# Performance work log

Hardware: AMD Instinct MI355X
Metric: run time of the kernel (lower is better)

The kernel has to match this reference:

```python
import jax, jax.numpy as jnp
import numpy as np

N_GROUPS = 32
N_HEADS = 16
EPS = 1e-5


def group_norm(x, w, b):
    # x: [B, C, T]
    B, C, T = x.shape
    xg = x.reshape(B, N_GROUPS, C // N_GROUPS, T)
    mu = xg.mean(axis=(2, 3), keepdims=True)
    var = xg.var(axis=(2, 3), keepdims=True)
    xn = ((xg - mu) * jax.lax.rsqrt(var + EPS)).reshape(B, C, T)
    return xn * w[None, :, None] + b[None, :, None]


def setup_inputs() -> dict:
    key = jax.random.key(0)
    ks = jax.random.split(key, 5)
    B, C, T = 4, 1024, 1024
    return {
        "x": jax.random.normal(ks[0], (B, C, T), jnp.float32),
        "norm_weight": jnp.ones((C,), jnp.float32),
        "norm_bias": jnp.zeros((C,), jnp.float32),
        "qkv_w": jax.random.normal(ks[1], (3 * C, C), jnp.float32) * 0.02,
        "qkv_b": jax.random.normal(ks[2], (3 * C,), jnp.float32) * 0.02,
        "proj_w": jax.random.normal(ks[3], (C, C), jnp.float32) * 0.02,
        "proj_b": jax.random.normal(ks[4], (C,), jnp.float32) * 0.02,
    }


def reference(x, norm_weight, norm_bias, qkv_w, qkv_b, proj_w, proj_b):
    B, C, T = x.shape
    H = N_HEADS
    ch = C // H
    # GroupNorm + 1x1 conv to QKV: [B, 3C, T]
    xn = group_norm(x, norm_weight, norm_bias)
    qkv = jnp.einsum('oc,bct->bot', qkv_w, xn) + qkv_b[None, :, None]
    # Legacy layout: [B, H*3*ch, T] -> [B, H, 3, ch, T]
    qkv = qkv.reshape(B, H, 3, ch, T)
    q, k, v = qkv[:, :, 0], qkv[:, :, 1], qkv[:, :, 2]
    scale = 1.0 / jnp.sqrt(jnp.sqrt(jnp.asarray(ch, x.dtype)))
    w = jnp.einsum('bhct,bhcs->bhts', q * scale, k * scale)
    w = jax.nn.softmax(w.astype(jnp.float32), axis=-1).astype(w.dtype)
    a = jnp.einsum('bhts,bhcs->bhct', w, v).reshape(B, C, T)
    h = jnp.einsum('oc,bct->bot', proj_w, a) + proj_b[None, :, None]
    return x + h
```

## Files before the change

### kernel.cpp

```cpp
#include <hip/hip_runtime.h>
#include <hip/hip_bf16.h>

typedef __bf16 bf16;
typedef bf16  bf16x4 __attribute__((ext_vector_type(4)));
typedef bf16  bf16x8 __attribute__((ext_vector_type(8)));
typedef float f32x4  __attribute__((ext_vector_type(4)));

union B8 { bf16x8 v; bf16 e[8]; };
union B4 { bf16x4 v; bf16 e[4]; };
union F4 { f32x4 v; float e[4]; };

#define GLOAD_LDS16(g, l)                                            \
  __builtin_amdgcn_global_load_lds(                                  \
      (const __attribute__((address_space(1))) void*)(g),            \
      (__attribute__((address_space(3))) void*)(l), 16, 0, 0)

#define SWZ(arr, R, c8) (*(const bf16x8*)&(arr)[(size_t)(R) * 64 + (((c8) ^ ((R) & 7)) << 3)])

__global__ __launch_bounds__(256) void conv_w_kernel(
    const float* __restrict__ qkvw, const float* __restrict__ qkvb,
    const float* __restrict__ pw,
    bf16* __restrict__ Wb, bf16* __restrict__ Pb, float* __restrict__ bs)
{
  const int row = blockIdx.x;
  const int tid = threadIdx.x;
  if (row < 3072) {
    const float s = ((row % 192) < 128) ? 0.42468158f : 1.0f;
    const float4 a = ((const float4*)(qkvw + (size_t)row * 1024))[tid];
    B4 o;
    o.e[0] = (bf16)(a.x * s); o.e[1] = (bf16)(a.y * s);
    o.e[2] = (bf16)(a.z * s); o.e[3] = (bf16)(a.w * s);
    ((bf16x4*)(Wb + (size_t)row * 1024))[tid] = o.v;
    if (tid == 0) bs[row] = qkvb[row] * s;
  } else {
    const int r = row - 3072;
    const float4 a = ((const float4*)(pw + (size_t)r * 1024))[tid];
    B4 o;
    o.e[0] = (bf16)a.x; o.e[1] = (bf16)a.y;
    o.e[2] = (bf16)a.z; o.e[3] = (bf16)a.w;
    ((bf16x4*)(Pb + (size_t)r * 1024))[tid] = o.v;
  }
}

__global__ __launch_bounds__(256) void gn_t_kernel(
    const float* __restrict__ x, const float* __restrict__ w,
    const float* __restrict__ bias, bf16* __restrict__ xnt)
{
  const int blk = blockIdx.x;
  const int b = blk >> 5, g = blk & 31;
  const float* xp = x + (size_t)(b * 1024 + g * 32) * 1024;
  const int tid = threadIdx.x;

  float s = 0.f, ss = 0.f;
  for (int ch = tid; ch < 4096; ch += 256) {
    const float4* p = (const float4*)(xp + (size_t)ch * 8);
    float4 u0 = p[0], u1 = p[1];
    s  += u0.x + u0.y + u0.z + u0.w + u1.x + u1.y + u1.z + u1.w;
    ss += u0.x*u0.x + u0.y*u0.y + u0.z*u0.z + u0.w*u0.w
        + u1.x*u1.x + u1.y*u1.y + u1.z*u1.z + u1.w*u1.w;
  }
  #pragma unroll
  for (int m = 1; m < 64; m <<= 1) { s += __shfl_xor(s, m); ss += __shfl_xor(ss, m); }

  __shared__ float red[8];
  __shared__ float stats[2];
  const int wave = tid >> 6, lane = tid & 63;
  if (lane == 0) { red[wave] = s; red[4 + wave] = ss; }
  __syncthreads();
  if (tid == 0) {
    float ts  = red[0] + red[1] + red[2] + red[3];
    float tss = red[4] + red[5] + red[6] + red[7];
    float mu  = ts * (1.f / 32768.f);
    float var = tss * (1.f / 32768.f) - mu * mu;
    stats[0] = mu;
    stats[1] = rsqrtf(var + 1e-5f);
  }
  __syncthreads();
  const float mu = stats[0], rs = stats[1];

  for (int ti = 0; ti < 4; ++ti) {
    const int t = ti * 256 + tid;
    B8 o[4];
    #pragma unroll
    for (int cc = 0; cc < 32; ++cc) {
      const float wt = w[g * 32 + cc] * rs;
      const float bsv = bias[g * 32 + cc];
      const float v = xp[(size_t)cc * 1024 + t];
      o[cc >> 3].e[cc & 7] = (bf16)((v - mu) * wt + bsv);
    }
    bf16* dst = xnt + (size_t)(b * 1024 + t) * 1024 + g * 32;
    #pragma unroll
    for (int j = 0; j < 4; ++j) *(bf16x8*)(dst + j * 8) = o[j].v;
  }
}

__global__ __launch_bounds__(256) void gemm_qkv_kernel(
    const bf16* __restrict__ xnt, const bf16* __restrict__ Wb,
    const float* __restrict__ bs, bf16* __restrict__ qkT, bf16* __restrict__ vv)
{
  const int bx = blockIdx.x;
  const int t0 = blockIdx.y * 128, z = blockIdx.z;
  const bf16* Ab = xnt + (size_t)z * 1024 * 1024;
  const bf16* Bb = Wb + (size_t)bx * 128 * 1024;

  __shared__ __align__(16) bf16 Al[128 * 64];
  __shared__ __align__(16) bf16 Bl[128 * 64];

  const int tid  = threadIdx.x;
  const int wave = tid >> 6, lane = tid & 63;
  const int quad = lane >> 4, l15 = lane & 15;
  const int wr = wave >> 1, wc = wave & 1;
  const int lrow = lane >> 3, lp = lane & 7;

  F4 acc[4][4];
  #pragma unroll
  for (int i = 0; i < 4; ++i)
    #pragma unroll
    for (int j = 0; j < 4; ++j) acc[i][j].v = (f32x4){0.f, 0.f, 0.f, 0.f};

  for (int k0 = 0; k0 < 1024; k0 += 64) {
    #pragma unroll
    for (int call = 0; call < 4; ++call) {
      const int row = wave * 32 + call * 8 + lrow;
      const int c8  = lp ^ (row & 7);
      GLOAD_LDS16(Ab + (size_t)(t0 + row) * 1024 + k0 + c8 * 8,
                  &Al[(wave * 32 + call * 8) * 64]);
      GLOAD_LDS16(Bb + (size_t)row * 1024 + k0 + c8 * 8,
                  &Bl[(wave * 32 + call * 8) * 64]);
    }
    __syncthreads();

    #pragma unroll
    for (int ks = 0; ks < 2; ++ks) {
      bf16x8 af[4], bfr[4];
      #pragma unroll
      for (int mt = 0; mt < 4; ++mt)
        af[mt] = SWZ(Al, wr * 64 + mt * 16 + l15, ks * 4 + quad);
      #pragma unroll
      for (int nt = 0; nt < 4; ++nt)
        bfr[nt] = SWZ(Bl, wc * 64 + nt * 16 + l15, ks * 4 + quad);
      #pragma unroll
      for (int mt = 0; mt < 4; ++mt)
        #pragma unroll
        for (int nt = 0; nt < 4; ++nt)
          acc[mt][nt].v = __builtin_amdgcn_mfma_f32_16x16x32_bf16(
              af[mt], bfr[nt], acc[mt][nt].v, 0, 0, 0);
    }
    __syncthreads();
  }

  #pragma unroll
  for (int nt = 0; nt < 4; ++nt) {
    const int base = bx * 128 + wc * 64 + nt * 16;
    const int r192 = base % 192, head = base / 192;
    const float bb = bs[base + l15];
    if (r192 < 128) {
      const size_t col = head * 128 + r192 + l15;
      #pragma unroll
      for (int mt = 0; mt < 4; ++mt)
        #pragma unroll
        for (int r = 0; r < 4; ++r) {
          const int t = t0 + wr * 64 + mt * 16 + quad * 4 + r;
          qkT[(size_t)(z * 1024 + t) * 2048 + col] = (bf16)(acc[mt][nt].e[r] + bb);
        }
    } else {
      bf16* vrow = vv + ((size_t)z * 1024 + head * 64 + (r192 - 128) + l15) * 1024;
      #pragma unroll
      for (int mt = 0; mt < 4; ++mt) {
        const int t = t0 + wr * 64 + mt * 16 + quad * 4;
        B4 pk;
        #pragma unroll
        for (int r = 0; r < 4; ++r) pk.e[r] = (bf16)(acc[mt][nt].e[r] + bb);
        *(bf16x4*)&vrow[t] = pk.v;
      }
    }
  }
}

__global__ __launch_bounds__(256) void gemm_proj_kernel(
    const bf16* __restrict__ Pb, const bf16* __restrict__ Bt,
    float* __restrict__ Cf, const float* __restrict__ bias,
    const float* __restrict__ resf)
{
  const int z = blockIdx.z;
  Bt   += (size_t)z * 1024 * 1024;
  Cf   += (size_t)z * 1024 * 1024;
  resf += (size_t)z * 1024 * 1024;
  const int n0 = blockIdx.x * 64, m0 = blockIdx.y * 64;

  __shared__ __align__(16) bf16 Al[64 * 64];
  __shared__ __align__(16) bf16 Bl[64 * 64];

  const int tid  = threadIdx.x;
  const int wave = tid >> 6, lane = tid & 63;
  const int quad = lane >> 4, l15 = lane & 15;
  const int wr = wave >> 1, wc = wave & 1;
  const int lrow = lane >> 3, lp = lane & 7;

  F4 acc[2][2];
  #pragma unroll
  for (int i = 0; i < 2; ++i)
    #pragma unroll
    for (int j = 0; j < 2; ++j) acc[i][j].v = (f32x4){0.f, 0.f, 0.f, 0.f};

  for (int k0 = 0; k0 < 1024; k0 += 64) {
    #pragma unroll
    for (int call = 0; call < 2; ++call) {
      const int row = wave * 16 + call * 8 + lrow;
      const int c8  = lp ^ (row & 7);
      GLOAD_LDS16(Pb + (size_t)(m0 + row) * 1024 + k0 + c8 * 8,
                  &Al[(wave * 16 + call * 8) * 64]);
      GLOAD_LDS16(Bt + (size_t)(n0 + row) * 1024 + k0 + c8 * 8,
                  &Bl[(wave * 16 + call * 8) * 64]);
    }
    __syncthreads();

    #pragma unroll
    for (int ks = 0; ks < 2; ++ks) {
      bf16x8 af[2], bfr[2];
      #pragma unroll
      for (int mt = 0; mt < 2; ++mt)
        af[mt] = SWZ(Al, wr * 32 + mt * 16 + l15, ks * 4 + quad);
      #pragma unroll
      for (int nt = 0; nt < 2; ++nt)
        bfr[nt] = SWZ(Bl, wc * 32 + nt * 16 + l15, ks * 4 + quad);
      #pragma unroll
      for (int mt = 0; mt < 2; ++mt)
        #pragma unroll
        for (int nt = 0; nt < 2; ++nt)
          acc[mt][nt].v = __builtin_amdgcn_mfma_f32_16x16x32_bf16(
              af[mt], bfr[nt], acc[mt][nt].v, 0, 0, 0);
    }
    __syncthreads();
  }

  #pragma unroll
  for (int mt = 0; mt < 2; ++mt) {
    #pragma unroll
    for (int r = 0; r < 4; ++r) {
      const int m = m0 + wr * 32 + mt * 16 + quad * 4 + r;
      const float bb = bias[m];
      #pragma unroll
      for (int nt = 0; nt < 2; ++nt) {
        const int n = n0 + wc * 32 + nt * 16 + l15;
        Cf[(size_t)m * 1024 + n] = acc[mt][nt].e[r] + bb + resf[(size_t)m * 1024 + n];
      }
    }
  }
}

__global__ __launch_bounds__(256) void attn_kernel(
    const bf16* __restrict__ qkTin, const bf16* __restrict__ vmat,
    bf16* __restrict__ aout)
{
  const int h = blockIdx.x, tt = blockIdx.y, z = blockIdx.z;
  const bf16* qk = qkTin + (size_t)z * 1024 * 2048;
  const bf16* vp = vmat + (size_t)z * 1024 * 1024 + (size_t)(h * 64) * 1024;
  aout += (size_t)z * 1024 * 1024;
  const int t0 = tt * 128;

  __shared__ __align__(16) bf16 qP[128 * 64];
  __shared__ __align__(16) bf16 kl[2][64 * 64];
  __shared__ __align__(16) bf16 vl[2][64 * 64];

  const int tid  = threadIdx.x;
  const int wave = tid >> 6, lane = tid & 63;
  const int quad = lane >> 4, l15 = lane & 15;
  const int lrow = lane >> 3, lp = lane & 7;

  #pragma unroll
  for (int c = 0; c < 4; ++c) {
    const int row = wave * 32 + c * 8 + lrow;
    const int c8  = lp ^ (row & 7);
    GLOAD_LDS16(qk + (size_t)(t0 + row) * 2048 + h * 128 + c8 * 8,
                &qP[(wave * 32 + c * 8) * 64]);
  }
  const int r0 = wave * 16 + lrow, r1 = wave * 16 + 8 + lrow;
  const int c80 = lp ^ (r0 & 7), c81 = lp ^ (r1 & 7);
  GLOAD_LDS16(qk + (size_t)r0 * 2048 + h * 128 + 64 + c80 * 8, &kl[0][(wave * 16) * 64]);
  GLOAD_LDS16(qk + (size_t)r1 * 2048 + h * 128 + 64 + c81 * 8, &kl[0][(wave * 16 + 8) * 64]);
  GLOAD_LDS16(vp + (size_t)r0 * 1024 + c80 * 8, &vl[0][(wave * 16) * 64]);
  GLOAD_LDS16(vp + (size_t)r1 * 1024 + c81 * 8, &vl[0][(wave * 16 + 8) * 64]);
  __syncthreads();

  bf16x8 bq0[2], bq1[2];
  int prow[2];
  #pragma unroll
  for (int b = 0; b < 2; ++b) {
    const int Rq = wave * 32 + b * 16 + l15;
    bq0[b] = SWZ(qP, Rq, quad);
    bq1[b] = SWZ(qP, Rq, quad + 4);
    prow[b] = Rq;
  }

  float l_i[2] = {0.f, 0.f};
  F4 oacc[2][4];
  #pragma unroll
  for (int b = 0; b < 2; ++b)
    #pragma unroll
    for (int ct = 0; ct < 4; ++ct) oacc[b][ct].v = (f32x4){0.f, 0.f, 0.f, 0.f};

  const int pq8 = (quad & 1) * 4;

  int buf = 0;
  for (int s0 = 0; s0 < 1024; s0 += 64) {
    if (s0 + 64 < 1024) {
      const int nb = buf ^ 1, sn = s0 + 64;
      GLOAD_LDS16(qk + (size_t)(sn + r0) * 2048 + h * 128 + 64 + c80 * 8,
                  &kl[nb][(wave * 16) * 64]);
      GLOAD_LDS16(qk + (size_t)(sn + r1) * 2048 + h * 128 + 64 + c81 * 8,
                  &kl[nb][(wave * 16 + 8) * 64]);
      GLOAD_LDS16(vp + (size_t)r0 * 1024 + sn + c80 * 8, &vl[nb][(wave * 16) * 64]);
      GLOAD_LDS16(vp + (size_t)r1 * 1024 + sn + c81 * 8, &vl[nb][(wave * 16 + 8) * 64]);
    }

    bf16x8 ak0[4], ak1[4], bv[2][4];
    #pragma unroll
    for (int st = 0; st < 4; ++st) {
      const int Rk = st * 16 + l15;
      ak0[st] = SWZ(kl[buf], Rk, quad);
      ak1[st] = SWZ(kl[buf], Rk, quad + 4);
    }
    #pragma unroll
    for (int ks = 0; ks < 2; ++ks)
      #pragma unroll
      for (int ct = 0; ct < 4; ++ct)
        bv[ks][ct] = SWZ(vl[buf], ct * 16 + l15, ks * 4 + quad);

    #pragma unroll
    for (int b = 0; b < 2; ++b) {
      F4 sacc[4];
      #pragma unroll
      for (int st = 0; st < 4; ++st) sacc[st].v = (f32x4){0.f, 0.f, 0.f, 0.f};
      #pragma unroll
      for (int st = 0; st < 4; ++st) {
        sacc[st].v = __builtin_amdgcn_mfma_f32_16x16x32_bf16(ak0[st], bq0[b], sacc[st].v, 0, 0, 0);
        sacc[st].v = __builtin_amdgcn_mfma_f32_16x16x32_bf16(ak1[st], bq1[b], sacc[st].v, 0, 0, 0);
      }

      bf16* const pbase = &qP[(size_t)prow[b] * 64];
      #pragma unroll
      for (int st = 0; st < 4; ++st) {
        B4 pk;
        #pragma unroll
        for (int r = 0; r < 4; ++r) {
          const float p = __builtin_amdgcn_exp2f(sacc[st].e[r]);
          l_i[b] += p;
          pk.e[r] = (bf16)p;
        }
        const int c8 = (st * 2 + (quad >> 1)) ^ (prow[b] & 7);
        *(bf16x4*)(pbase + (c8 << 3) + pq8) = pk.v;
      }

      #pragma unroll
      for (int ks = 0; ks < 2; ++ks) {
        const bf16x8 ap = SWZ(qP, prow[b], ks * 4 + quad);
        #pragma unroll
        for (int ct = 0; ct < 4; ++ct)
          oacc[b][ct].v = __builtin_amdgcn_mfma_f32_16x16x32_bf16(
              ap, bv[ks][ct], oacc[b][ct].v, 0, 0, 0);
      }
    }
    __syncthreads();
    buf ^= 1;
  }

  #pragma unroll
  for (int b = 0; b < 2; ++b) {
    float li = l_i[b];
    li += __shfl_xor(li, 16);
    li += __shfl_xor(li, 32);
    const float inv = 1.f / li;
    float iv[4];
    #pragma unroll
    for (int r = 0; r < 4; ++r) iv[r] = __shfl(inv, quad * 4 + r);
    #pragma unroll
    for (int r = 0; r < 4; ++r) {
      const int t = t0 + wave * 32 + b * 16 + quad * 4 + r;
      #pragma unroll
      for (int ct = 0; ct < 4; ++ct)
        aout[(size_t)t * 1024 + h * 64 + ct * 16 + l15] = (bf16)(oacc[b][ct].e[r] * iv[r]);
    }
  }
}

extern "C" void kernel_launch(void* const* d_in, const int* in_sizes, int n_in,
                              void* d_out, int out_size, void* d_ws, size_t ws_size,
                              hipStream_t stream)
{
  const float* x    = (const float*)d_in[0];
  const float* nw   = (const float*)d_in[1];
  const float* nb   = (const float*)d_in[2];
  const float* qkvw = (const float*)d_in[3];
  const float* qkvb = (const float*)d_in[4];
  const float* pw   = (const float*)d_in[5];
  const float* pb   = (const float*)d_in[6];
  float* out = (float*)d_out;

  const long M1 = 1024L * 1024L;
  bf16*  xnt = (bf16*)d_ws;
  bf16*  qkT = xnt + 4 * M1;
  bf16*  vv  = xnt + 12 * M1;
  bf16*  at  = xnt + 16 * M1;
  bf16*  Wb  = xnt + 20 * M1;
  bf16*  Pb  = xnt + 23 * M1;
  float* bs  = (float*)(xnt + 24 * M1);

  conv_w_kernel<<<dim3(4096), dim3(256), 0, stream>>>(qkvw, qkvb, pw, Wb, Pb, bs);
  gn_t_kernel<<<dim3(128), dim3(256), 0, stream>>>(x, nw, nb, xnt);
  gemm_qkv_kernel<<<dim3(24, 8, 4), dim3(256), 0, stream>>>(xnt, Wb, bs, qkT, vv);
  attn_kernel<<<dim3(16, 8, 4), dim3(256), 0, stream>>>(qkT, vv, at);
  gemm_proj_kernel<<<dim3(16, 16, 4), dim3(256), 0, stream>>>(Pb, at, out, pb, x);
}
```

Baseline: 185.8 us.

## Rewrite QKV GEMM with 256x256 tiles, double-buffered LDS and phased prefetch

The QKV projection GEMM moves from 128x128 tiles with 4 waves and a single LDS buffer to 256x256 tiles with 8 waves, two LDS buffers and a hand-scheduled four-phase loop. Global-to-LDS loads for the next K steps are interleaved with MFMA work, using explicit vmcnt waits, barriers and setprio. Blocks are remapped onto a flat grid with a swizzle so neighbouring blocks share tiles in L2. This aims to hide load latency and improve data reuse, but it uses more LDS and registers per block and produces only 192 blocks, so occupancy is lower and the CUs may not all be kept busy.

```diff
diff --git a/kernel.cpp b/kernel.cpp
--- a/kernel.cpp
+++ b/kernel.cpp
@@ -94,84 +94,128 @@
   }
 }
 
-__global__ __launch_bounds__(256) void gemm_qkv_kernel(
+__global__ __launch_bounds__(512, 2) void gemm_qkv_kernel(
     const bf16* __restrict__ xnt, const bf16* __restrict__ Wb,
     const float* __restrict__ bs, bf16* __restrict__ qkT, bf16* __restrict__ vv)
 {
-  const int bx = blockIdx.x;
-  const int t0 = blockIdx.y * 128, z = blockIdx.z;
-  const bf16* Ab = xnt + (size_t)z * 1024 * 1024;
-  const bf16* Bb = Wb + (size_t)bx * 128 * 1024;
-
-  __shared__ __align__(16) bf16 Al[128 * 64];
-  __shared__ __align__(16) bf16 Bl[128 * 64];
+  const int bid = blockIdx.x;
+  const int swz = (bid & 7) * 24 + (bid >> 3);
+  const int bxn = swz % 12, bym = swz / 12;
+  const int n0 = bxn * 256, m0 = bym * 256;
+
+  __shared__ __align__(16) bf16 Al[2][256 * 64];
+  __shared__ __align__(16) bf16 Bl[2][256 * 64];
 
   const int tid  = threadIdx.x;
   const int wave = tid >> 6, lane = tid & 63;
   const int quad = lane >> 4, l15 = lane & 15;
-  const int wr = wave >> 1, wc = wave & 1;
+  const int wr = wave >> 2, wc = wave & 3;
   const int lrow = lane >> 3, lp = lane & 7;
-
-  F4 acc[4][4];
-  #pragma unroll
-  for (int i = 0; i < 4; ++i)
+  const int sc8 = (lp ^ lrow) << 3;
+
+  #define STAGE_A(bufn, kt, c)                                               \
+    GLOAD_LDS16(xnt + (size_t)(m0 + (c) * 64 + wave * 8 + lrow) * 1024 +     \
+                    (kt) * 64 + sc8,                                         \
+                &Al[bufn][((c) * 64 + wave * 8) * 64])
+  #define STAGE_B(bufn, kt, c)                                               \
+    GLOAD_LDS16(Wb + (size_t)(n0 + (c) * 64 + wave * 8 + lrow) * 1024 +      \
+                    (kt) * 64 + sc8,                                         \
+                &Bl[bufn][((c) * 64 + wave * 8) * 64])
+
+  F4 acc[8][4];
+  #pragma unroll
+  for (int i = 0; i < 8; ++i)
     #pragma unroll
     for (int j = 0; j < 4; ++j) acc[i][j].v = (f32x4){0.f, 0.f, 0.f, 0.f};
 
-  for (int k0 = 0; k0 < 1024; k0 += 64) {
-    #pragma unroll
-    for (int call = 0; call < 4; ++call) {
-      const int row = wave * 32 + call * 8 + lrow;
-      const int c8  = lp ^ (row & 7);
-      GLOAD_LDS16(Ab + (size_t)(t0 + row) * 1024 + k0 + c8 * 8,
-                  &Al[(wave * 32 + call * 8) * 64]);
-      GLOAD_LDS16(Bb + (size_t)row * 1024 + k0 + c8 * 8,
-                  &Bl[(wave * 32 + call * 8) * 64]);
-    }
-    __syncthreads();
-
-    #pragma unroll
-    for (int ks = 0; ks < 2; ++ks) {
-      bf16x8 af[4], bfr[4];
-      #pragma unroll
-      for (int mt = 0; mt < 4; ++mt)
-        af[mt] = SWZ(Al, wr * 64 + mt * 16 + l15, ks * 4 + quad);
-      #pragma unroll
-      for (int nt = 0; nt < 4; ++nt)
-        bfr[nt] = SWZ(Bl, wc * 64 + nt * 16 + l15, ks * 4 + quad);
-      #pragma unroll
-      for (int mt = 0; mt < 4; ++mt)
-        #pragma unroll
-        for (int nt = 0; nt < 4; ++nt)
-          acc[mt][nt].v = __builtin_amdgcn_mfma_f32_16x16x32_bf16(
-              af[mt], bfr[nt], acc[mt][nt].v, 0, 0, 0);
-    }
-    __syncthreads();
-  }
+  #pragma unroll
+  for (int c = 0; c < 4; ++c) STAGE_A(0, 0, c);
+  #pragma unroll
+  for (int c = 0; c < 4; ++c) STAGE_B(0, 0, c);
+  #pragma unroll
+  for (int c = 0; c < 4; ++c) STAGE_B(1, 1, c);
+  STAGE_A(1, 1, 0); STAGE_A(1, 1, 2);
+  asm volatile("s_waitcnt vmcnt(6)" ::: "memory");
+  __builtin_amdgcn_s_barrier();
+  asm volatile("" ::: "memory");
+
+  bf16x8 bfrag[2][4];
+
+  for (int t = 0; t < 16; ++t) {
+    const int cb = t & 1, nb = cb ^ 1;
+    #pragma unroll
+    for (int ph = 0; ph < 4; ++ph) {
+      if (ph == 0) {
+        #pragma unroll
+        for (int kk = 0; kk < 2; ++kk)
+          #pragma unroll
+          for (int nt = 0; nt < 4; ++nt)
+            bfrag[kk][nt] = SWZ(Bl[cb], wc * 64 + nt * 16 + l15, kk * 4 + quad);
+      }
+      bf16x8 af[2][2];
+      #pragma unroll
+      for (int i = 0; i < 2; ++i)
+        #pragma unroll
+        for (int kk = 0; kk < 2; ++kk)
+          af[i][kk] = SWZ(Al[cb], wr * 128 + (2 * ph + i) * 16 + l15, kk * 4 + quad);
+
+      if (ph == 0 && t + 1 < 16) { STAGE_A(nb, t + 1, 1); STAGE_A(nb, t + 1, 3); }
+      if (ph == 1 && t + 2 < 16) { STAGE_B(cb, t + 2, 0); STAGE_B(cb, t + 2, 1); }
+      if (ph == 2 && t + 2 < 16) { STAGE_B(cb, t + 2, 2); STAGE_B(cb, t + 2, 3); }
+      if (ph == 3 && t + 2 < 16) { STAGE_A(cb, t + 2, 0); STAGE_A(cb, t + 2, 2); }
+
+      asm volatile("" ::: "memory");
+      __builtin_amdgcn_s_barrier();
+      asm volatile("s_waitcnt lgkmcnt(0)" ::: "memory");
+      __builtin_amdgcn_sched_barrier(0);
+
+      __builtin_amdgcn_s_setprio(1);
+      #pragma unroll
+      for (int kk = 0; kk < 2; ++kk)
+        #pragma unroll
+        for (int i = 0; i < 2; ++i)
+          #pragma unroll
+          for (int nt = 0; nt < 4; ++nt)
+            acc[2 * ph + i][nt].v = __builtin_amdgcn_mfma_f32_16x16x32_bf16(
+                af[i][kk], bfrag[kk][nt], acc[2 * ph + i][nt].v, 0, 0, 0);
+      __builtin_amdgcn_s_setprio(0);
+
+      if (ph == 3) {
+        if (t < 14)       asm volatile("s_waitcnt vmcnt(6)" ::: "memory");
+        else if (t == 14) asm volatile("s_waitcnt vmcnt(0)" ::: "memory");
+      }
+      asm volatile("" ::: "memory");
+      __builtin_amdgcn_s_barrier();
+      asm volatile("" ::: "memory");
+    }
+  }
+  #undef STAGE_A
+  #undef STAGE_B
 
   #pragma unroll
   for (int nt = 0; nt < 4; ++nt) {
-    const int base = bx * 128 + wc * 64 + nt * 16;
+    const int base = n0 + wc * 64 + nt * 16;
     const int r192 = base % 192, head = base / 192;
     const float bb = bs[base + l15];
     if (r192 < 128) {
-      const size_t col = head * 128 + r192 + l15;
-      #pragma unroll
-      for (int mt = 0; mt < 4; ++mt)
+      const int col = head * 128 + r192 + l15;
+      #pragma unroll
+      for (int mt = 0; mt < 8; ++mt)
         #pragma unroll
         for (int r = 0; r < 4; ++r) {
-          const int t = t0 + wr * 64 + mt * 16 + quad * 4 + r;
-          qkT[(size_t)(z * 1024 + t) * 2048 + col] = (bf16)(acc[mt][nt].e[r] + bb);
+          const int m = m0 + wr * 128 + mt * 16 + quad * 4 + r;
+          qkT[(size_t)m * 2048 + col] = (bf16)(acc[mt][nt].e[r] + bb);
         }
     } else {
+      const int z = m0 >> 10;
       bf16* vrow = vv + ((size_t)z * 1024 + head * 64 + (r192 - 128) + l15) * 1024;
-      #pragma unroll
-      for (int mt = 0; mt < 4; ++mt) {
-        const int t = t0 + wr * 64 + mt * 16 + quad * 4;
+      const int tb = (m0 & 1023) + wr * 128;
+      #pragma unroll
+      for (int mt = 0; mt < 8; ++mt) {
         B4 pk;
         #pragma unroll
         for (int r = 0; r < 4; ++r) pk.e[r] = (bf16)(acc[mt][nt].e[r] + bb);
-        *(bf16x4*)&vrow[t] = pk.v;
+        *(bf16x4*)&vrow[tb + mt * 16 + quad * 4] = pk.v;
       }
     }
   }
@@ -408,7 +452,7 @@
 
   conv_w_kernel<<<dim3(4096), dim3(256), 0, stream>>>(qkvw, qkvb, pw, Wb, Pb, bs);
   gn_t_kernel<<<dim3(128), dim3(256), 0, stream>>>(x, nw, nb, xnt);
-  gemm_qkv_kernel<<<dim3(24, 8, 4), dim3(256), 0, stream>>>(xnt, Wb, bs, qkT, vv);
+  gemm_qkv_kernel<<<dim3(192), dim3(512), 0, stream>>>(xnt, Wb, bs, qkT, vv);
   attn_kernel<<<dim3(16, 8, 4), dim3(256), 0, stream>>>(qkT, vv, at);
   gemm_proj_kernel<<<dim3(16, 16, 4), dim3(256), 0, stream>>>(Pb, at, out, pb, x);
 }
```

After: 190.8 us. 2.7% more time.

## Retile QKV GEMM to 256x192 double-buffered tiles with block swizzle

Applied to the files above, without the earlier changes.

Rewrites the QKV projection GEMM to use 512-thread blocks computing 256x192 output tiles, one head per column tile, with a flat 256-block grid and a grouped block-index swizzle. Global-to-LDS loads for the next K step are issued into a second buffer while MFMAs run on the current one, which drops one barrier per iteration and overlaps memory with compute. Larger tiles raise operand reuse and cut redundant global reads. The cost is much more LDS (about 112 KB) and many more accumulator registers, which limits occupancy. The 256-block grid may also leave some compute units idle.

```diff
diff --git a/kernel.cpp b/kernel.cpp
--- a/kernel.cpp
+++ b/kernel.cpp
@@ -94,84 +94,100 @@
   }
 }
 
-__global__ __launch_bounds__(256) void gemm_qkv_kernel(
+__global__ __launch_bounds__(512, 2) void gemm_qkv_kernel(
     const bf16* __restrict__ xnt, const bf16* __restrict__ Wb,
     const float* __restrict__ bs, bf16* __restrict__ qkT, bf16* __restrict__ vv)
 {
-  const int bx = blockIdx.x;
-  const int t0 = blockIdx.y * 128, z = blockIdx.z;
-  const bf16* Ab = xnt + (size_t)z * 1024 * 1024;
-  const bf16* Bb = Wb + (size_t)bx * 128 * 1024;
-
-  __shared__ __align__(16) bf16 Al[128 * 64];
-  __shared__ __align__(16) bf16 Bl[128 * 64];
+  const int bid = blockIdx.x;
+  const int swz = (bid & 7) * 32 + (bid >> 3);
+  const int bxn = swz >> 4, bym = swz & 15;
+  const int n0 = bxn * 192, m0 = bym * 256;
+  const int head = bxn;
+
+  __shared__ __align__(16) bf16 Al[2][256 * 64];
+  __shared__ __align__(16) bf16 Bl[2][192 * 64];
 
   const int tid  = threadIdx.x;
   const int wave = tid >> 6, lane = tid & 63;
   const int quad = lane >> 4, l15 = lane & 15;
-  const int wr = wave >> 1, wc = wave & 1;
+  const int wr = wave >> 2, wc = wave & 3;
   const int lrow = lane >> 3, lp = lane & 7;
-
-  F4 acc[4][4];
-  #pragma unroll
-  for (int i = 0; i < 4; ++i)
-    #pragma unroll
-    for (int j = 0; j < 4; ++j) acc[i][j].v = (f32x4){0.f, 0.f, 0.f, 0.f};
-
-  for (int k0 = 0; k0 < 1024; k0 += 64) {
-    #pragma unroll
-    for (int call = 0; call < 4; ++call) {
-      const int row = wave * 32 + call * 8 + lrow;
-      const int c8  = lp ^ (row & 7);
-      GLOAD_LDS16(Ab + (size_t)(t0 + row) * 1024 + k0 + c8 * 8,
-                  &Al[(wave * 32 + call * 8) * 64]);
-      GLOAD_LDS16(Bb + (size_t)row * 1024 + k0 + c8 * 8,
-                  &Bl[(wave * 32 + call * 8) * 64]);
-    }
+  const int sc8 = (lp ^ lrow) << 3;
+
+  #define STAGE(bufn, kt) do {                                                \
+    _Pragma("unroll")                                                         \
+    for (int c = 0; c < 4; ++c)                                               \
+      GLOAD_LDS16(xnt + (size_t)(m0 + c * 64 + wave * 8 + lrow) * 1024 +      \
+                      (size_t)(kt) * 64 + sc8,                                \
+                  &Al[bufn][(c * 64 + wave * 8) * 64]);                       \
+    _Pragma("unroll")                                                         \
+    for (int c = 0; c < 3; ++c)                                               \
+      GLOAD_LDS16(Wb + (size_t)(n0 + c * 64 + wave * 8 + lrow) * 1024 +       \
+                      (size_t)(kt) * 64 + sc8,                                \
+                  &Bl[bufn][(c * 64 + wave * 8) * 64]);                       \
+  } while (0)
+
+  F4 acc[8][3];
+  #pragma unroll
+  for (int i = 0; i < 8; ++i)
+    #pragma unroll
+    for (int j = 0; j < 3; ++j) acc[i][j].v = (f32x4){0.f, 0.f, 0.f, 0.f};
+
+  STAGE(0, 0);
+  __syncthreads();
+
+  for (int t = 0; t < 16; ++t) {
+    const int cb = t & 1;
+
+    bf16x8 af[2][8], bfr[2][3];
+    #pragma unroll
+    for (int kk = 0; kk < 2; ++kk) {
+      #pragma unroll
+      for (int nt = 0; nt < 3; ++nt)
+        bfr[kk][nt] = SWZ(Bl[cb], wc * 48 + nt * 16 + l15, kk * 4 + quad);
+      #pragma unroll
+      for (int mt = 0; mt < 8; ++mt)
+        af[kk][mt] = SWZ(Al[cb], wr * 128 + mt * 16 + l15, kk * 4 + quad);
+    }
+
+    if (t + 1 < 16) STAGE(cb ^ 1, t + 1);
+
+    #pragma unroll
+    for (int kk = 0; kk < 2; ++kk)
+      #pragma unroll
+      for (int mt = 0; mt < 8; ++mt)
+        #pragma unroll
+        for (int nt = 0; nt < 3; ++nt)
+          acc[mt][nt].v = __builtin_amdgcn_mfma_f32_16x16x32_bf16(
+              af[kk][mt], bfr[kk][nt], acc[mt][nt].v, 0, 0, 0);
+
     __syncthreads();
-
-    #pragma unroll
-    for (int ks = 0; ks < 2; ++ks) {
-      bf16x8 af[4], bfr[4];
-      #pragma unroll
-      for (int mt = 0; mt < 4; ++mt)
-        af[mt] = SWZ(Al, wr * 64 + mt * 16 + l15, ks * 4 + quad);
-      #pragma unroll
-      for (int nt = 0; nt < 4; ++nt)
-        bfr[nt] = SWZ(Bl, wc * 64 + nt * 16 + l15, ks * 4 + quad);
-      #pragma unroll
-      for (int mt = 0; mt < 4; ++mt)
-        #pragma unroll
-        for (int nt = 0; nt < 4; ++nt)
-          acc[mt][nt].v = __builtin_amdgcn_mfma_f32_16x16x32_bf16(
-              af[mt], bfr[nt], acc[mt][nt].v, 0, 0, 0);
-    }
-    __syncthreads();
-  }
-
-  #pragma unroll
-  for (int nt = 0; nt < 4; ++nt) {
-    const int base = bx * 128 + wc * 64 + nt * 16;
-    const int r192 = base % 192, head = base / 192;
-    const float bb = bs[base + l15];
+  }
+  #undef STAGE
+
+  const int z  = m0 >> 10;
+  const int tb = (m0 & 1023) + wr * 128;
+  #pragma unroll
+  for (int nt = 0; nt < 3; ++nt) {
+    const int r192 = wc * 48 + nt * 16;
+    const float bb = bs[n0 + r192 + l15];
     if (r192 < 128) {
-      const size_t col = head * 128 + r192 + l15;
-      #pragma unroll
-      for (int mt = 0; mt < 4; ++mt)
+      const int col = head * 128 + r192 + l15;
+      #pragma unroll
+      for (int mt = 0; mt < 8; ++mt)
         #pragma unroll
         for (int r = 0; r < 4; ++r) {
-          const int t = t0 + wr * 64 + mt * 16 + quad * 4 + r;
-          qkT[(size_t)(z * 1024 + t) * 2048 + col] = (bf16)(acc[mt][nt].e[r] + bb);
+          const int m = m0 + wr * 128 + mt * 16 + quad * 4 + r;
+          qkT[(size_t)m * 2048 + col] = (bf16)(acc[mt][nt].e[r] + bb);
         }
     } else {
       bf16* vrow = vv + ((size_t)z * 1024 + head * 64 + (r192 - 128) + l15) * 1024;
       #pragma unroll
-      for (int mt = 0; mt < 4; ++mt) {
-        const int t = t0 + wr * 64 + mt * 16 + quad * 4;
+      for (int mt = 0; mt < 8; ++mt) {
         B4 pk;
         #pragma unroll
         for (int r = 0; r < 4; ++r) pk.e[r] = (bf16)(acc[mt][nt].e[r] + bb);
-        *(bf16x4*)&vrow[t] = pk.v;
+        *(bf16x4*)&vrow[tb + mt * 16 + quad * 4] = pk.v;
       }
     }
   }
@@ -408,7 +424,7 @@
 
   conv_w_kernel<<<dim3(4096), dim3(256), 0, stream>>>(qkvw, qkvb, pw, Wb, Pb, bs);
   gn_t_kernel<<<dim3(128), dim3(256), 0, stream>>>(x, nw, nb, xnt);
-  gemm_qkv_kernel<<<dim3(24, 8, 4), dim3(256), 0, stream>>>(xnt, Wb, bs, qkT, vv);
+  gemm_qkv_kernel<<<dim3(256), dim3(512), 0, stream>>>(xnt, Wb, bs, qkT, vv);
   attn_kernel<<<dim3(16, 8, 4), dim3(256), 0, stream>>>(qkT, vv, at);
   gemm_proj_kernel<<<dim3(16, 16, 4), dim3(256), 0, stream>>>(Pb, at, out, pb, x);
 }
```

Result: faster. 176.1 us (-5.2%).
